# Kernel tuning notes

Measured on AMD Instinct MI355X. Metric: run time of the kernel, lower is better.

Reference implementation:

```python
import jax, jax.numpy as jnp
import numpy as np

N_NODES = 100000
N_EDGES = 3200000
LEAKY_SLOPE = 0.01  # torch nn.LeakyReLU default


def setup_inputs() -> dict:
    key = jax.random.key(0)
    ks = jax.random.split(key, 9)
    x = jax.random.normal(ks[0], (N_NODES, 128), dtype=jnp.float32)
    edge_index = jax.random.randint(ks[1], (2, N_EDGES), 0, N_NODES, dtype=jnp.int64)
    weights = jax.random.uniform(ks[2], (N_EDGES,), dtype=jnp.float32)
    # GCNConv linear weights (glorot-ish init) and biases
    def lin(k, fin, fout):
        s = (6.0 / (fin + fout)) ** 0.5
        return jax.random.uniform(k, (fout, fin), dtype=jnp.float32, minval=-s, maxval=s)
    W1 = lin(ks[3], 128, 64); b1 = jnp.zeros((64,), jnp.float32)
    W2 = lin(ks[4], 64, 32);  b2 = jnp.zeros((32,), jnp.float32)
    W3 = lin(ks[5], 32, 4);   b3 = jnp.zeros((4,), jnp.float32)
    return {"x_embeddings": x, "edge_index": edge_index, "weights": weights,
            "W1": W1, "b1": b1, "W2": W2, "b2": b2, "W3": W3, "b3": b3}


def _gcn_norm(src, dst, weights, n_nodes):
    # PyG gcn_norm with add_self_loops=True, fill_value=1
    loop = jnp.arange(n_nodes, dtype=src.dtype)
    src_a = jnp.concatenate([src, loop])
    dst_a = jnp.concatenate([dst, loop])
    w_a = jnp.concatenate([weights, jnp.ones((n_nodes,), weights.dtype)])
    deg = jax.ops.segment_sum(w_a, dst_a, num_segments=n_nodes)
    dis = jnp.where(deg > 0, jax.lax.rsqrt(jnp.where(deg > 0, deg, 1.0)), 0.0)
    norm = dis[src_a] * w_a * dis[dst_a]
    return src_a, dst_a, norm


def _gcn_conv(x, W, b, src_a, dst_a, norm, n_nodes):
    h = x @ W.T                              # [N, fout]
    msg = norm[:, None] * h[src_a]           # [E+N, fout] gather
    out = jax.ops.segment_sum(msg, dst_a, num_segments=n_nodes)  # scatter-add
    return out + b


def reference(x_embeddings, edge_index, weights, W1, b1, W2, b2, W3, b3):
    n = x_embeddings.shape[0]
    src, dst = edge_index[0], edge_index[1]
    src_a, dst_a, norm = _gcn_norm(src, dst, weights, n)
    # eval mode: F.dropout(training=False) is identity
    h = _gcn_conv(x_embeddings, W1, b1, src_a, dst_a, norm, n)
    h = jax.nn.leaky_relu(h, LEAKY_SLOPE)
    h = _gcn_conv(h, W2, b2, src_a, dst_a, norm, n)
    h = jax.nn.leaky_relu(h, LEAKY_SLOPE)
    h = _gcn_conv(h, W3, b3, src_a, dst_a, norm, n)
    return jax.nn.softmax(h, axis=1)
```

## Files before the change

kernel.cpp:

```cpp
#include <hip/hip_runtime.h>
#include <hip/hip_fp16.h>


#define BLK 256

__global__ __launch_bounds__(256) void k_hist(const int* __restrict__ dst,
                                              int* __restrict__ hist,
                                              int E, int CH, int NB) {
    __shared__ int h[256];
    int b = blockIdx.x, t = threadIdx.x;
    h[t] = 0;
    __syncthreads();
    int beg = b * CH, fin = min(E, beg + CH);
    for (int e = beg + t; e < fin; e += 256)
        atomicAdd(&h[dst[e] >> 9], 1);
    __syncthreads();
    if (t < NB) hist[t * 256 + b] = h[t];
}

__global__ void k_scan1(const int* __restrict__ in, int* __restrict__ outv,
                        int* __restrict__ partials, int n) {
    __shared__ int sm[256];
    int i = blockIdx.x * 256 + threadIdx.x;
    int v = (i < n) ? in[i] : 0;
    sm[threadIdx.x] = v;
    __syncthreads();
    for (int off = 1; off < 256; off <<= 1) {
        int t = (threadIdx.x >= off) ? sm[threadIdx.x - off] : 0;
        __syncthreads();
        sm[threadIdx.x] += t;
        __syncthreads();
    }
    if (i < n) outv[i] = sm[threadIdx.x] - v;
    if (threadIdx.x == 255) partials[blockIdx.x] = sm[255];
}

__global__ void k_scan2(int* __restrict__ partials, int nb) {
    __shared__ int sm[512];
    int t = threadIdx.x;
    int v = (t < nb) ? partials[t] : 0;
    sm[t] = v;
    __syncthreads();
    for (int off = 1; off < 512; off <<= 1) {
        int x = (t >= off) ? sm[t - off] : 0;
        __syncthreads();
        sm[t] += x;
        __syncthreads();
    }
    if (t < nb) partials[t] = sm[t] - v;
}

__global__ void k_scan3(int* __restrict__ data, const int* __restrict__ partials, int n) {
    int i = blockIdx.x * 256 + threadIdx.x;
    if (i < n) data[i] += partials[i >> 8];
}

__global__ __launch_bounds__(256) void k_bscatter(const int* __restrict__ src,
                                                  const int* __restrict__ dst,
                                                  const float* __restrict__ w,
                                                  const int* __restrict__ scanout,
                                                  int2* __restrict__ tmp,
                                                  int E, int CH, int NB) {
    __shared__ int cur[256];
    int b = blockIdx.x, t = threadIdx.x;
    if (t < NB) cur[t] = scanout[t * 256 + b];
    __syncthreads();
    int beg = b * CH, fin = min(E, beg + CH);
    for (int e = beg + t; e < fin; e += 256) {
        int d = dst[e];
        int q = d >> 9;
        int pos = atomicAdd(&cur[q], 1);
        tmp[pos] = make_int2(((d & 511) << 18) | src[e], __float_as_int(w[e]));
    }
}

__global__ __launch_bounds__(256) void k_bcsr(const int* __restrict__ scanout,
                                              const int2* __restrict__ tmp,
                                              int2* __restrict__ pack,
                                              int* __restrict__ row_ptr,
                                              float* __restrict__ dis,
                                              int n, int E, int NB) {
    __shared__ int cnt[512];
    __shared__ float wsum[512];
    __shared__ int psum[256];
    int q = blockIdx.x, t = threadIdx.x;
    int base = scanout[q * 256];
    int end  = (q == NB - 1) ? E : scanout[(q + 1) * 256];
    cnt[t] = 0; cnt[t + 256] = 0;
    wsum[t] = 0.f; wsum[t + 256] = 0.f;
    __syncthreads();
    for (int j = base + t; j < end; j += 256) {
        int2 r = tmp[j];
        int d = r.x >> 18;
        atomicAdd(&cnt[d], 1);
        atomicAdd(&wsum[d], __int_as_float(r.y));
    }
    __syncthreads();
    int a = cnt[2 * t], bb = cnt[2 * t + 1];
    psum[t] = a + bb;
    __syncthreads();
    for (int off = 1; off < 256; off <<= 1) {
        int v = (t >= off) ? psum[t - off] : 0;
        __syncthreads();
        psum[t] += v;
        __syncthreads();
    }
    int pex = psum[t] - (a + bb);
    __syncthreads();
    cnt[2 * t] = pex;
    cnt[2 * t + 1] = pex + a;
    int node0 = q * 512;
    if (node0 + 2 * t < n) {
        row_ptr[node0 + 2 * t] = base + pex;
        dis[node0 + 2 * t] = rsqrtf(1.f + wsum[2 * t]);
    }
    if (node0 + 2 * t + 1 < n) {
        row_ptr[node0 + 2 * t + 1] = base + pex + a;
        dis[node0 + 2 * t + 1] = rsqrtf(1.f + wsum[2 * t + 1]);
    }
    if (q == 0 && t == 0) row_ptr[n] = E;
    __syncthreads();
    for (int j = base + t; j < end; j += 256) {
        int2 r = tmp[j];
        int d = r.x >> 18;
        int pos = base + atomicAdd(&cnt[d], 1);
        pack[pos] = make_int2(r.x & 0x3FFFF, r.y);
    }
}

__global__ __launch_bounds__(256) void k_norm(const int* __restrict__ rp,
                                              const float* __restrict__ dis,
                                              int2* __restrict__ pack, int n) {
    int node = blockIdx.x * 4 + (threadIdx.x >> 6);
    int lane = threadIdx.x & 63;
    if (node >= n) return;
    float dd = dis[node];
    int beg = rp[node], end = rp[node + 1];
    for (int j = beg + lane; j < end; j += 64) {
        int2 p = pack[j];
        p.y = __float_as_int(dd * __int_as_float(p.y) * dis[p.x]);
        pack[j] = p;
    }
}

__device__ __forceinline__ float leaky01(float v) {
    return v > 0.f ? v : 0.01f * v;
}
__device__ __forceinline__ float h2f(ushort u) {
    return __half2float(__ushort_as_half(u));
}
__device__ __forceinline__ ushort f2h(float f) {
    return __half_as_ushort(__float2half(f));
}
__device__ __forceinline__ float2 h2f2(uint u) {
    return make_float2(h2f((ushort)(u & 0xffff)), h2f((ushort)(u >> 16)));
}

__global__ __launch_bounds__(256) void k_linear1(
        const float* __restrict__ in, const float* __restrict__ W,
        ushort* __restrict__ outh, int n) {
    constexpr int FIN = 128, FOUT = 64, TM = 64, CPT = 16;
    constexpr int WS = 68;
    constexpr int XS = TM + 1;
    __shared__ __align__(16) float Wt[FIN * WS];
    __shared__ __align__(16) float xst[FIN * XS];
    const int tid = threadIdx.x;
    const int nb = blockIdx.x * TM;

    for (int i = tid; i < FIN * FOUT; i += 256) {
        int c = i >> 7, k = i & 127;
        Wt[k * WS + c] = W[i];
    }
    __syncthreads();
    for (int i4 = tid; i4 < TM * FIN / 4; i4 += 256) {
        int idx = i4 * 4;
        int r = idx >> 7, k0 = idx & 127;
        if (nb + r < n) {
            float4 v = *(const float4*)&in[(size_t)(nb + r) * FIN + k0];
            xst[(k0 + 0) * XS + r] = v.x;
            xst[(k0 + 1) * XS + r] = v.y;
            xst[(k0 + 2) * XS + r] = v.z;
            xst[(k0 + 3) * XS + r] = v.w;
        }
    }
    __syncthreads();

    const int nl = tid >> 2;
    const int c0 = (tid & 3) * CPT;
    if (nb + nl >= n) return;

    float4 acc[CPT / 4];
#pragma unroll
    for (int j = 0; j < CPT / 4; ++j) acc[j] = make_float4(0.f, 0.f, 0.f, 0.f);
#pragma unroll 8
    for (int k = 0; k < FIN; ++k) {
        float xv = xst[k * XS + nl];
        const float4* wr = (const float4*)&Wt[k * WS + c0];
#pragma unroll
        for (int j = 0; j < CPT / 4; ++j) {
            float4 w4 = wr[j];
            acc[j].x += xv * w4.x; acc[j].y += xv * w4.y;
            acc[j].z += xv * w4.z; acc[j].w += xv * w4.w;
        }
    }
    uint* o = (uint*)&outh[(size_t)(nb + nl) * FOUT + c0];
#pragma unroll
    for (int j = 0; j < CPT / 4; ++j) {
        float4 a = acc[j];
        o[2 * j + 0] = (uint)f2h(a.x) | ((uint)f2h(a.y) << 16);
        o[2 * j + 1] = (uint)f2h(a.z) | ((uint)f2h(a.w) << 16);
    }
}

__global__ __launch_bounds__(256) void fgather64(
        const int* __restrict__ rp, const int2* __restrict__ pack,
        const float* __restrict__ dis, const ushort* __restrict__ h1h,
        const float* __restrict__ b1, const float* __restrict__ W2,
        ushort* __restrict__ h2h, int n) {
    __shared__ float sW2t[64 * 33];
    __shared__ float sact[4][64];
    int tid = threadIdx.x;
    for (int i = tid; i < 2048; i += 256)
        sW2t[(i & 63) * 33 + (i >> 6)] = W2[i];
    int w = tid >> 6, l = tid & 63;
    int es = l >> 3, g = l & 7;
    int node = blockIdx.x * 4 + w;
    bool valid = node < n;
    float acc[8] = {0.f, 0.f, 0.f, 0.f, 0.f, 0.f, 0.f, 0.f};
    if (valid) {
        int beg = rp[node], end = rp[node + 1];
        int j = beg;
        for (; j + 16 <= end; j += 16) {
            int2 pa = pack[j + es];
            int2 pb = pack[j + 8 + es];
            uint4 ua = *(const uint4*)&h1h[(size_t)pa.x * 64 + 8 * g];
            uint4 ub = *(const uint4*)&h1h[(size_t)pb.x * 64 + 8 * g];
            float na = __int_as_float(pa.y), nb2 = __int_as_float(pb.y);
            float2 v;
            v = h2f2(ua.x); acc[0] += na * v.x;  acc[1] += na * v.y;
            v = h2f2(ua.y); acc[2] += na * v.x;  acc[3] += na * v.y;
            v = h2f2(ua.z); acc[4] += na * v.x;  acc[5] += na * v.y;
            v = h2f2(ua.w); acc[6] += na * v.x;  acc[7] += na * v.y;
            v = h2f2(ub.x); acc[0] += nb2 * v.x; acc[1] += nb2 * v.y;
            v = h2f2(ub.y); acc[2] += nb2 * v.x; acc[3] += nb2 * v.y;
            v = h2f2(ub.z); acc[4] += nb2 * v.x; acc[5] += nb2 * v.y;
            v = h2f2(ub.w); acc[6] += nb2 * v.x; acc[7] += nb2 * v.y;
        }
        for (; j < end; j += 8) {
            if (j + es < end) {
                int2 p = pack[j + es];
                uint4 u = *(const uint4*)&h1h[(size_t)p.x * 64 + 8 * g];
                float nm = __int_as_float(p.y);
                float2 v;
                v = h2f2(u.x); acc[0] += nm * v.x; acc[1] += nm * v.y;
                v = h2f2(u.y); acc[2] += nm * v.x; acc[3] += nm * v.y;
                v = h2f2(u.z); acc[4] += nm * v.x; acc[5] += nm * v.y;
                v = h2f2(u.w); acc[6] += nm * v.x; acc[7] += nm * v.y;
            }
        }
#pragma unroll
        for (int u = 0; u < 8; ++u) {
            acc[u] += __shfl_xor(acc[u], 8);
            acc[u] += __shfl_xor(acc[u], 16);
            acc[u] += __shfl_xor(acc[u], 32);
        }
        if (es == 0) {
            float dd = dis[node], d2 = dd * dd;
            uint4 u = *(const uint4*)&h1h[(size_t)node * 64 + 8 * g];
            float2 v;
            v = h2f2(u.x); acc[0] += d2 * v.x; acc[1] += d2 * v.y;
            v = h2f2(u.y); acc[2] += d2 * v.x; acc[3] += d2 * v.y;
            v = h2f2(u.z); acc[4] += d2 * v.x; acc[5] += d2 * v.y;
            v = h2f2(u.w); acc[6] += d2 * v.x; acc[7] += d2 * v.y;
#pragma unroll
            for (int u2 = 0; u2 < 8; ++u2)
                sact[w][8 * g + u2] = leaky01(acc[u2] + b1[8 * g + u2]);
        }
    }
    __syncthreads();
    if (valid) {
        int c2 = l & 31, half = l >> 5;
        float s = 0.f;
#pragma unroll 8
        for (int cc = 0; cc < 32; ++cc) {
            int c = half * 32 + cc;
            s += sW2t[c * 33 + c2] * sact[w][c];
        }
        s += __shfl_xor(s, 32);
        if (l < 32) h2h[(size_t)node * 32 + c2] = f2h(s);
    }
}

__global__ __launch_bounds__(256) void fgather32(
        const int* __restrict__ rp, const int2* __restrict__ pack,
        const float* __restrict__ dis, const ushort* __restrict__ h2h,
        const float* __restrict__ b2, const float* __restrict__ W3,
        float* __restrict__ h3out, int n) {
    __shared__ float sW3t[32 * 5];
    __shared__ float sact[4][32];
    int tid = threadIdx.x;
    if (tid < 128) sW3t[(tid & 31) * 5 + (tid >> 5)] = W3[tid];
    int w = tid >> 6, l = tid & 63;
    int es = l >> 3, g = l & 7;
    int node = blockIdx.x * 4 + w;
    bool valid = node < n;
    float acc[4] = {0.f, 0.f, 0.f, 0.f};
    if (valid) {
        int beg = rp[node], end = rp[node + 1];
        int j = beg;
        for (; j + 16 <= end; j += 16) {
            int2 pa = pack[j + es];
            int2 pb = pack[j + 8 + es];
            uint2 ua = *(const uint2*)&h2h[(size_t)pa.x * 32 + 4 * g];
            uint2 ub = *(const uint2*)&h2h[(size_t)pb.x * 32 + 4 * g];
            float na = __int_as_float(pa.y), nb2 = __int_as_float(pb.y);
            float2 v;
            v = h2f2(ua.x); acc[0] += na * v.x;  acc[1] += na * v.y;
            v = h2f2(ua.y); acc[2] += na * v.x;  acc[3] += na * v.y;
            v = h2f2(ub.x); acc[0] += nb2 * v.x; acc[1] += nb2 * v.y;
            v = h2f2(ub.y); acc[2] += nb2 * v.x; acc[3] += nb2 * v.y;
        }
        for (; j < end; j += 8) {
            if (j + es < end) {
                int2 p = pack[j + es];
                uint2 u = *(const uint2*)&h2h[(size_t)p.x * 32 + 4 * g];
                float nm = __int_as_float(p.y);
                float2 v;
                v = h2f2(u.x); acc[0] += nm * v.x; acc[1] += nm * v.y;
                v = h2f2(u.y); acc[2] += nm * v.x; acc[3] += nm * v.y;
            }
        }
#pragma unroll
        for (int u = 0; u < 4; ++u) {
            acc[u] += __shfl_xor(acc[u], 8);
            acc[u] += __shfl_xor(acc[u], 16);
            acc[u] += __shfl_xor(acc[u], 32);
        }
        if (es == 0) {
            float dd = dis[node], d2 = dd * dd;
            uint2 u = *(const uint2*)&h2h[(size_t)node * 32 + 4 * g];
            float2 v;
            v = h2f2(u.x); acc[0] += d2 * v.x; acc[1] += d2 * v.y;
            v = h2f2(u.y); acc[2] += d2 * v.x; acc[3] += d2 * v.y;
#pragma unroll
            for (int u2 = 0; u2 < 4; ++u2)
                sact[w][4 * g + u2] = leaky01(acc[u2] + b2[4 * g + u2]);
        }
    }
    __syncthreads();
    if (valid && l < 32) {
        int c3 = l & 3;
        float s = 0.f;
#pragma unroll
        for (int m = 0; m < 4; ++m) {
            int c = (l >> 2) + 8 * m;
            s += sW3t[c * 5 + c3] * sact[w][c];
        }
        s += __shfl_xor(s, 4, 32);
        s += __shfl_xor(s, 8, 32);
        s += __shfl_xor(s, 16, 32);
        if (l < 4) h3out[(size_t)node * 4 + l] = s;
    }
}

__global__ __launch_bounds__(256) void fgather4(
        const int* __restrict__ rp, const int2* __restrict__ pack,
        const float* __restrict__ dis, const float* __restrict__ h3,
        const float* __restrict__ b3, float* __restrict__ out, int n) {
    int tid = threadIdx.x;
    int node = blockIdx.x * 8 + (tid >> 5);
    int l32 = tid & 31;
    if (node >= n) return;
    int beg = rp[node], end = rp[node + 1];
    float4 acc = make_float4(0.f, 0.f, 0.f, 0.f);
    for (int j = beg + l32; j < end; j += 32) {
        int2 p = pack[j];
        float4 hr = *(const float4*)&h3[(size_t)p.x * 4];
        float nm = __int_as_float(p.y);
        acc.x += nm * hr.x; acc.y += nm * hr.y;
        acc.z += nm * hr.z; acc.w += nm * hr.w;
    }
#pragma unroll
    for (int off = 1; off <= 16; off <<= 1) {
        acc.x += __shfl_xor(acc.x, off, 32);
        acc.y += __shfl_xor(acc.y, off, 32);
        acc.z += __shfl_xor(acc.z, off, 32);
        acc.w += __shfl_xor(acc.w, off, 32);
    }
    if (l32 == 0) {
        float dd = dis[node], d2 = dd * dd;
        float4 hr = *(const float4*)&h3[(size_t)node * 4];
        float v0 = acc.x + d2 * hr.x + b3[0];
        float v1 = acc.y + d2 * hr.y + b3[1];
        float v2 = acc.z + d2 * hr.z + b3[2];
        float v3 = acc.w + d2 * hr.w + b3[3];
        float m = fmaxf(fmaxf(v0, v1), fmaxf(v2, v3));
        float e0 = expf(v0 - m), e1 = expf(v1 - m);
        float e2 = expf(v2 - m), e3 = expf(v3 - m);
        float inv = 1.f / (e0 + e1 + e2 + e3);
        *(float4*)&out[(size_t)node * 4] =
            make_float4(e0 * inv, e1 * inv, e2 * inv, e3 * inv);
    }
}

static inline int cdiv(long long a, int b) { return (int)((a + b - 1) / b); }

extern "C" void kernel_launch(void* const* d_in, const int* in_sizes, int n_in,
                              void* d_out, int out_size, void* d_ws, size_t ws_size,
                              hipStream_t stream) {
    const float* x   = (const float*)d_in[0];
    const int*   ei  = (const int*)d_in[1];
    const float* ew  = (const float*)d_in[2];
    const float* W1  = (const float*)d_in[3];
    const float* b1  = (const float*)d_in[4];
    const float* W2  = (const float*)d_in[5];
    const float* b2  = (const float*)d_in[6];
    const float* W3  = (const float*)d_in[7];
    const float* b3  = (const float*)d_in[8];
    float* out = (float*)d_out;

    const int N = in_sizes[0] / 128;
    const int E = in_sizes[2];
    const int* src = ei;
    const int* dst = ei + E;

    const int NB = (N + 511) >> 9;
    const int GB = 256;
    const int CH = cdiv(E, GB);
    const int n_scan = NB * GB;

    char* base = (char*)d_ws;
    auto alloc = [&](size_t bytes) {
        char* p = base;
        base += (bytes + 255) & ~(size_t)255;
        return p;
    };
    float* dis      = (float*)alloc((size_t)N * 4);
    int*   row_ptr  = (int*)  alloc(((size_t)N + 1) * 4);
    int*   hist     = (int*)  alloc((size_t)n_scan * 4);
    int*   scanout  = (int*)  alloc((size_t)n_scan * 4);
    int*   partials = (int*)  alloc(512 * 4);
    int2*  pack     = (int2*) alloc((size_t)E * 8);
    char*  regA     = alloc((size_t)N * 64 * 4);
    char*  regB     = alloc((size_t)N * 64 * 4);
    int2*   tmp = (int2*)regA;
    ushort* h1h = (ushort*)regA;
    float*  h3  = (float*)regA;
    ushort* h2h = (ushort*)regB;

    k_hist<<<GB, 256, 0, stream>>>(dst, hist, E, CH, NB);
    k_scan1<<<cdiv(n_scan, 256), 256, 0, stream>>>(hist, scanout, partials, n_scan);
    k_scan2<<<1, 512, 0, stream>>>(partials, cdiv(n_scan, 256));
    k_scan3<<<cdiv(n_scan, 256), 256, 0, stream>>>(scanout, partials, n_scan);
    k_bscatter<<<GB, 256, 0, stream>>>(src, dst, ew, scanout, tmp, E, CH, NB);
    k_bcsr<<<NB, 256, 0, stream>>>(scanout, tmp, pack, row_ptr, dis, N, E, NB);
    k_norm<<<cdiv(N, 4), 256, 0, stream>>>(row_ptr, dis, pack, N);

    k_linear1<<<cdiv(N, 64), 256, 0, stream>>>(x, W1, h1h, N);
    fgather64<<<cdiv(N, 4), 256, 0, stream>>>(row_ptr, pack, dis, h1h, b1, W2, h2h, N);
    fgather32<<<cdiv(N, 4), 256, 0, stream>>>(row_ptr, pack, dis, h2h, b2, W3, h3, N);
    fgather4<<<cdiv(N, 8), 256, 0, stream>>>(row_ptr, pack, dis, h3, b3, out, N);
}
```

Measured before the change: 351.4 us.

## Use MFMA fp16 matrix instructions for the first linear layer

Rewrites the 128->64 linear kernel to use the CDNA 16x16x32 fp16 MFMA instruction. Each wave computes 16 rows by loading fp32 inputs directly from global memory and converting them to fp16, with W held as fp16 in shared memory. This replaces the scalar FMA loop and the transposed input staging in LDS. Inputs are now rounded to fp16 before the multiply, which lowers precision, and the output stores are scattered 2-byte writes.

```diff
diff --git a/kernel.cpp b/kernel.cpp
--- a/kernel.cpp
+++ b/kernel.cpp
@@ -3,6 +3,9 @@
 
 
 #define BLK 256
+
+typedef _Float16 f16x8 __attribute__((ext_vector_type(8)));
+typedef float f32x4 __attribute__((ext_vector_type(4)));
 
 __global__ __launch_bounds__(256) void k_hist(const int* __restrict__ dst,
                                               int* __restrict__ hist,
@@ -159,56 +162,46 @@
 __global__ __launch_bounds__(256) void k_linear1(
         const float* __restrict__ in, const float* __restrict__ W,
         ushort* __restrict__ outh, int n) {
-    constexpr int FIN = 128, FOUT = 64, TM = 64, CPT = 16;
-    constexpr int WS = 68;
-    constexpr int XS = TM + 1;
-    __shared__ __align__(16) float Wt[FIN * WS];
-    __shared__ __align__(16) float xst[FIN * XS];
-    const int tid = threadIdx.x;
-    const int nb = blockIdx.x * TM;
-
-    for (int i = tid; i < FIN * FOUT; i += 256) {
+    constexpr int WS = 136;
+    __shared__ _Float16 sW[64 * WS];
+    int tid = threadIdx.x;
+    for (int i = tid; i < 8192; i += 256) {
         int c = i >> 7, k = i & 127;
-        Wt[k * WS + c] = W[i];
-    }
-    __syncthreads();
-    for (int i4 = tid; i4 < TM * FIN / 4; i4 += 256) {
-        int idx = i4 * 4;
-        int r = idx >> 7, k0 = idx & 127;
-        if (nb + r < n) {
-            float4 v = *(const float4*)&in[(size_t)(nb + r) * FIN + k0];
-            xst[(k0 + 0) * XS + r] = v.x;
-            xst[(k0 + 1) * XS + r] = v.y;
-            xst[(k0 + 2) * XS + r] = v.z;
-            xst[(k0 + 3) * XS + r] = v.w;
-        }
-    }
-    __syncthreads();
-
-    const int nl = tid >> 2;
-    const int c0 = (tid & 3) * CPT;
-    if (nb + nl >= n) return;
-
-    float4 acc[CPT / 4];
-#pragma unroll
-    for (int j = 0; j < CPT / 4; ++j) acc[j] = make_float4(0.f, 0.f, 0.f, 0.f);
-#pragma unroll 8
-    for (int k = 0; k < FIN; ++k) {
-        float xv = xst[k * XS + nl];
-        const float4* wr = (const float4*)&Wt[k * WS + c0];
-#pragma unroll
-        for (int j = 0; j < CPT / 4; ++j) {
-            float4 w4 = wr[j];
-            acc[j].x += xv * w4.x; acc[j].y += xv * w4.y;
-            acc[j].z += xv * w4.z; acc[j].w += xv * w4.w;
-        }
-    }
-    uint* o = (uint*)&outh[(size_t)(nb + nl) * FOUT + c0];
-#pragma unroll
-    for (int j = 0; j < CPT / 4; ++j) {
-        float4 a = acc[j];
-        o[2 * j + 0] = (uint)f2h(a.x) | ((uint)f2h(a.y) << 16);
-        o[2 * j + 1] = (uint)f2h(a.z) | ((uint)f2h(a.w) << 16);
+        sW[c * WS + k] = (_Float16)W[i];
+    }
+    __syncthreads();
+    int w = tid >> 6, l = tid & 63;
+    int lr = l & 15, lg = l >> 4;
+    int row0 = blockIdx.x * 64 + w * 16;
+    if (row0 >= n) return;
+    int arow = min(row0 + lr, n - 1);
+    const float* xr = in + (size_t)arow * 128 + lg * 8;
+
+    f32x4 acc[4] = {{0.f,0.f,0.f,0.f},{0.f,0.f,0.f,0.f},
+                    {0.f,0.f,0.f,0.f},{0.f,0.f,0.f,0.f}};
+#pragma unroll
+    for (int kt = 0; kt < 4; ++kt) {
+        float4 a0 = *(const float4*)(xr + kt * 32);
+        float4 a1 = *(const float4*)(xr + kt * 32 + 4);
+        f16x8 af;
+        af[0] = (_Float16)a0.x; af[1] = (_Float16)a0.y;
+        af[2] = (_Float16)a0.z; af[3] = (_Float16)a0.w;
+        af[4] = (_Float16)a1.x; af[5] = (_Float16)a1.y;
+        af[6] = (_Float16)a1.z; af[7] = (_Float16)a1.w;
+#pragma unroll
+        for (int ct = 0; ct < 4; ++ct) {
+            int c = ct * 16 + lr;
+            f16x8 bf = *(const f16x8*)&sW[c * WS + kt * 32 + lg * 8];
+            acc[ct] = __builtin_amdgcn_mfma_f32_16x16x32_f16(af, bf, acc[ct], 0, 0, 0);
+        }
+    }
+#pragma unroll
+    for (int ct = 0; ct < 4; ++ct) {
+#pragma unroll
+        for (int i = 0; i < 4; ++i) {
+            int r = row0 + lg * 4 + i;
+            if (r < n) outh[(size_t)r * 64 + ct * 16 + lr] = f2h(acc[ct][i]);
+        }
     }
 }
 
```

New measurement: 312.1 us. -11.2%, faster.
